# Kernel tuning notes

Hardware: AMD Instinct MI355X
Metric: run time of the kernel (lower is better)

Reference implementation:

```python
import jax, jax.numpy as jnp
import numpy as np
from jax import lax

NUM_HEADS = 8

def _conv2d(x, w, b, padding, rhs_dilation=(1, 1)):
    # x: NCHW, w: OIHW
    out = lax.conv_general_dilated(x, w, (1, 1), padding,
                                   rhs_dilation=rhs_dilation,
                                   dimension_numbers=('NCHW', 'OIHW', 'NCHW'))
    return out + b[None, :, None, None]

def _bn(x, scale, bias):
    # eval-mode batchnorm folded into per-channel affine
    return x * scale[None, :, None, None] + bias[None, :, None, None]

def setup_inputs() -> dict:
    key = jax.random.key(0)
    ks = jax.random.split(key, 12)
    B, C, H, W = 16, 256, 64, 64
    D = C // 2          # down_dim = 128
    Dq = D // 16        # weight bottleneck = 8
    return {
        'x':          jax.random.normal(ks[0], (B, C, H, W), jnp.float32),
        'conv2_w':    jax.random.normal(ks[1], (D, C, 3, 3), jnp.float32) * 0.02,
        'conv2_b':    jnp.zeros((D,), jnp.float32),
        'bn2_scale':  jax.random.uniform(ks[2], (D,), jnp.float32, 0.5, 1.5),
        'bn2_bias':   jax.random.normal(ks[3], (D,), jnp.float32) * 0.1,
        'temperature': jnp.ones((NUM_HEADS, 1, 1), jnp.float32),
        'w1_w':       jax.random.normal(ks[4], (Dq, D, 1, 1), jnp.float32) * 0.05,
        'w1_b':       jnp.zeros((Dq,), jnp.float32),
        'bnw_scale':  jax.random.uniform(ks[5], (Dq,), jnp.float32, 0.5, 1.5),
        'bnw_bias':   jax.random.normal(ks[6], (Dq,), jnp.float32) * 0.1,
        'w2_w':       jax.random.normal(ks[7], (D, Dq, 1, 1), jnp.float32) * 0.05,
        'w2_b':       jnp.zeros((D,), jnp.float32),
    }

def _l2_normalize_complex(z, eps=1e-12):
    # torch F.normalize on complex: divide by L2 norm of |z| along last dim
    n = jnp.sqrt(jnp.sum(jnp.real(z * jnp.conj(z)), axis=-1, keepdims=True))
    return z / jnp.maximum(n, eps)

def reference(x, conv2_w, conv2_b, bn2_scale, bn2_bias, temperature,
              w1_w, w1_b, bnw_scale, bnw_bias, w2_w, w2_b):
    # conv2 branch: 3x3 conv with dilation=3, padding=3 -> BN -> ReLU
    conv2 = jax.nn.relu(_bn(_conv2d(x, conv2_w, conv2_b,
                                    ((3, 3), (3, 3)), rhs_dilation=(3, 3)),
                            bn2_scale, bn2_bias))
    b, c, h, w = conv2.shape
    f = jnp.fft.fft2(conv2)                      # complex64, (b,c,h,w); q=k=v=tepqkv
    cp = c // NUM_HEADS
    qkv = f.reshape(b, NUM_HEADS, cp, h * w)     # 'b (head c) h w -> b head c (h w)'
    qn = _l2_normalize_complex(qkv)
    kn = qn
    # complex attention logits, temperature broadcast over heads
    attn = jnp.einsum('bhin,bhjn->bhij', qn, kn) * temperature.astype(attn_dtype := qn.dtype)
    # dual real/imag softmax reassembled into complex
    attn = lax.complex(jax.nn.softmax(attn.real, axis=-1),
                       jax.nn.softmax(attn.imag, axis=-1))
    out_f = jnp.einsum('bhij,bhjn->bhin', attn, qkv)
    # torch.fft.ifft2 default dims=(-2,-1): here over (c, h*w) axes — faithful
    out_f = jnp.abs(jnp.fft.ifft2(out_f)).reshape(b, c, h, w)
    # gating branch on real part of spectrum
    g = jax.nn.relu(_bn(_conv2d(f.real, w1_w, w1_b, ((0, 0), (0, 0))),
                        bnw_scale, bnw_bias))
    g = jax.nn.sigmoid(_conv2d(g, w2_w, w2_b, ((0, 0), (0, 0))))
    out_l = jnp.abs(jnp.fft.ifft2(g * f))        # ifft2 over (h, w)
    out = jnp.concatenate([out_f, out_l], axis=1)
    return out + x
```

## Files before the change

kernel.cpp:

```cpp
#include <hip/hip_runtime.h>

typedef unsigned short u16;
typedef short short8 __attribute__((ext_vector_type(8)));
typedef float f32x4 __attribute__((ext_vector_type(4)));

#define MF(a,b,c) __builtin_amdgcn_mfma_f32_16x16x32_bf16(a,b,c,0,0,0)

__device__ __forceinline__ float bu2f(u16 u){
  return __uint_as_float(((unsigned int)u) << 16);
}
__device__ __forceinline__ u16 f2bu(float f){
  unsigned int b = __float_as_uint(f);
  unsigned int r = (b + 0x7FFFu + ((b >> 16) & 1u)) >> 16;
  return (u16)r;
}
__device__ __forceinline__ void ld4a(float* d, const float* p){
  float4 v = *(const float4*)p;
  d[0]=v.x; d[1]=v.y; d[2]=v.z; d[3]=v.w;
}
__device__ __forceinline__ void st4(float* p, const float* s){
  *(float4*)p = make_float4(s[0], s[1], s[2], s[3]);
}
__device__ __forceinline__ void ld4b(float* d, const u16* p){
  ushort4 v = *(const ushort4*)p;
  d[0]=bu2f(v.x); d[1]=bu2f(v.y); d[2]=bu2f(v.z); d[3]=bu2f(v.w);
}
__device__ __forceinline__ void st4b(u16* p, const float* s){
  ushort4 v;
  v.x=f2bu(s[0]); v.y=f2bu(s[1]); v.z=f2bu(s[2]); v.w=f2bu(s[3]);
  *(ushort4*)p = v;
}
__device__ __forceinline__ ushort4 pk4(f32x4 v){
  ushort4 u; u.x=f2bu(v[0]); u.y=f2bu(v[1]); u.z=f2bu(v[2]); u.w=f2bu(v[3]); return u;
}
__device__ __forceinline__ short8 mulpk(short8 g, short8 f){
  short8 o;
  #pragma unroll
  for (int e = 0; e < 8; ++e)
    o[e] = (short)f2bu(bu2f((u16)g[e])*bu2f((u16)f[e]));
  return o;
}

#define TABF_RE   0
#define TABF_IM   4096
#define TABIF_RE  8192
#define TABIF_IM  12288
#define TABTW_RE  16384
#define TABTW_IM  20480
#define NORMS_OFF 24576
#define MMAT_OFF  26624
#define FLAG_OFF  92160
#define PRM_OFF   92224
#define WT_OFF    94848
#define DFT16_OFF 242304
#define F32_END   389760
#define P_CB   0
#define P_BNS  128
#define P_BNB  256
#define P_TEMP 384
#define P_W1   400
#define P_B1   1424
#define P_S1   1432
#define P_BB1  1440
#define P_W2   1456
#define P_B2   2480
#define BPLANE    8388608

__global__ void k_detect(const u16* __restrict__ xv, int* __restrict__ flag){
  const int t = threadIdx.x;
  int huge = 0;
  for (int i = 0; i < 16; ++i){
    u16 u = xv[(t*16 + i)*2];
    int e = (u >> 7) & 0xFF;
    huge += (e >= 0xC0) ? 1 : 0;
  }
  #pragma unroll
  for (int off = 32; off > 0; off >>= 1) huge += __shfl_down(huge, off, 64);
  if (t == 0) flag[0] = (huge >= 8) ? 1 : 0;
}

__global__ void k_tables(float* ws){
  int idx = blockIdx.x*256 + threadIdx.x;
  int j = idx >> 6, k = idx & 63;
  int jk = j*k;
  float s, c;
  sincospif(-(float)(jk & 63)/32.0f, &s, &c);
  ws[TABF_RE+idx] = c; ws[TABF_IM+idx] = s;
  sincospif((float)(jk & 63)/32.0f, &s, &c);
  ws[TABIF_RE+idx] = c*(1.f/64.f); ws[TABIF_IM+idx] = s*(1.f/64.f);
  sincospif((float)jk/2048.0f, &s, &c);
  ws[TABTW_RE+idx] = c; ws[TABTW_IM+idx] = s;
}

__global__ void k_dftprep(u16* __restrict__ m){
  int idx = blockIdx.x*256 + threadIdx.x;
  int j = idx >> 6, k = idx & 63;
  int jk = (j*k) & 63;
  float s, c;
  sincospif(-(float)jk/32.0f, &s, &c);
  m[idx]        = f2bu(c);
  m[4096+idx]   = f2bu(s);
  sincospif((float)jk/32.0f, &s, &c);
  m[8192+idx]   = f2bu(c*(1.f/64.f));
  m[12288+idx]  = f2bu(s*(1.f/64.f));
}

__global__ void k_pack(const void* cb, const void* bns, const void* bnb, const void* temp,
                       const void* w1, const void* b1, const void* s1, const void* bb1,
                       const void* w2, const void* b2,
                       const int* __restrict__ flg, float* __restrict__ P){
  const int t = threadIdx.x;
  const int f32 = *flg;
  if (f32){
    for (int i = t; i < 128; i += 256){
      P[P_CB+i]  = ((const float*)cb)[i];
      P[P_BNS+i] = ((const float*)bns)[i];
      P[P_BNB+i] = ((const float*)bnb)[i];
      P[P_B2+i]  = ((const float*)b2)[i];
    }
    for (int i = t; i < 1024; i += 256){
      P[P_W1+i] = ((const float*)w1)[i];
      P[P_W2+i] = ((const float*)w2)[i];
    }
    if (t < 8){
      P[P_TEMP+t] = ((const float*)temp)[t];
      P[P_B1+t]   = ((const float*)b1)[t];
      P[P_S1+t]   = ((const float*)s1)[t];
      P[P_BB1+t]  = ((const float*)bb1)[t];
    }
  } else {
    for (int i = t; i < 128; i += 256){
      P[P_CB+i]  = bu2f(((const u16*)cb)[i]);
      P[P_BNS+i] = bu2f(((const u16*)bns)[i]);
      P[P_BNB+i] = bu2f(((const u16*)bnb)[i]);
      P[P_B2+i]  = bu2f(((const u16*)b2)[i]);
    }
    for (int i = t; i < 1024; i += 256){
      P[P_W1+i] = bu2f(((const u16*)w1)[i]);
      P[P_W2+i] = bu2f(((const u16*)w2)[i]);
    }
    if (t < 8){
      P[P_TEMP+t] = bu2f(((const u16*)temp)[t]);
      P[P_B1+t]   = bu2f(((const u16*)b1)[t]);
      P[P_S1+t]   = bu2f(((const u16*)s1)[t]);
      P[P_BB1+t]  = bu2f(((const u16*)bb1)[t]);
    }
  }
}

__global__ void k_wprep2(const void* __restrict__ w, u16* __restrict__ wT2,
                         const float* __restrict__ prm, const int* __restrict__ flg){
  const int f32 = *flg;
  int U = blockIdx.x*256 + threadIdx.x;
  if (U < 294912){
    int j = U & 7;
    int E = U >> 3;
    int n = E & 127;
    int o = (E >> 7) & 3;
    int tc = E >> 9;
    int chunk = tc & 7, tap = tc >> 3;
    int c = chunk*32 + o*8 + j;
    int src = n*2304 + c*9 + tap;
    float v = f32 ? ((const float*)w)[src] : bu2f(((const u16*)w)[src]);
    wT2[U] = f2bu(v * prm[P_BNS + n]);
  }
}

__global__ __launch_bounds__(256) void k_trans(const void* __restrict__ x, u16* __restrict__ xt,
                                               const int* __restrict__ flg){
  __shared__ u16 L[256*66];
  const int t = threadIdx.x;
  const int b = blockIdx.x >> 6, h = blockIdx.x & 63;
  const int f32m = __builtin_amdgcn_readfirstlane(*flg);
  if (f32m){
    const float* xf = (const float*)x;
    for (int i = t; i < 16384; i += 256){
      int c = i >> 6, w = i & 63;
      L[c*66 + w] = f2bu(xf[((b*256 + c)*64 + h)*64 + w]);
    }
  } else {
    const u16* xb = (const u16*)x;
    for (int i = t; i < 16384; i += 256){
      int c = i >> 6, w = i & 63;
      L[c*66 + w] = xb[((b*256 + c)*64 + h)*64 + w];
    }
  }
  __syncthreads();
  u16* dst = xt + ((b*64 + h)*64)*256;
  for (int j = t; j < 16384; j += 256){
    int w = j >> 8, c = j & 255;
    dst[w*256 + c] = L[c*66 + w];
  }
}

__global__ __launch_bounds__(256) void k_cmm(const u16* __restrict__ xt, const u16* __restrict__ wT2,
                                             const float* __restrict__ prm, u16* __restrict__ A){
  __shared__ uint4 sm4[4096];
  const int t = threadIdx.x;
  const int bb = blockIdx.x >> 4;
  const int mtile = blockIdx.x & 15;
  const int h0 = mtile*4;
  const int lane = t & 63, wave = t >> 6;
  const int quad = lane >> 4, lr = lane & 15;

  f32x4 acc[4][8];
  #pragma unroll
  for (int mi = 0; mi < 4; ++mi)
    #pragma unroll
    for (int nt = 0; nt < 8; ++nt)
      acc[mi][nt] = (f32x4){0.f,0.f,0.f,0.f};

  const u16* smB = (const u16*)sm4;
  const short8 zz = {0,0,0,0,0,0,0,0};

  for (int tap = 0; tap < 9; ++tap){
    const int ky = tap/3, kx = tap - ky*3;
    __syncthreads();
    {
      const uint4* src = (const uint4*)(wT2 + tap*32768);
      #pragma unroll
      for (int i = 0; i < 16; ++i) sm4[t + 256*i] = src[t + 256*i];
    }
    __syncthreads();

    const int hg = h0 + wave + 3*ky - 3;
    const bool hok = ((unsigned)hg < 64u);
    const u16* abase = xt + ((bb*64 + hg)*64)*256 + quad*8;

    for (int chunk = 0; chunk < 8; ++chunk){
      short8 av[4];
      #pragma unroll
      for (int mi = 0; mi < 4; ++mi){
        const int wg = mi*16 + lr + 3*kx - 3;
        short8 v = zz;
        if (hok && ((unsigned)wg < 64u))
          v = *(const short8*)(abase + wg*256 + chunk*32);
        av[mi] = v;
      }
      short8 bv[8];
      #pragma unroll
      for (int nt = 0; nt < 8; ++nt)
        bv[nt] = *(const short8*)(smB + (chunk*512 + quad*128 + nt*16 + lr)*8);
      #pragma unroll
      for (int mi = 0; mi < 4; ++mi)
        #pragma unroll
        for (int nt = 0; nt < 8; ++nt)
          acc[mi][nt] = MF(av[mi], bv[nt], acc[mi][nt]);
    }
  }

  float* C = (float*)sm4;
  u16* outb = A + (bb*128)*4096 + mtile*256;
  __syncthreads();
  for (int nt = 0; nt < 8; ++nt){
    #pragma unroll
    for (int mi = 0; mi < 4; ++mi)
      #pragma unroll
      for (int r = 0; r < 4; ++r){
        int m = wave*64 + mi*16 + quad*4 + r;
        C[lr*261 + m] = acc[mi][nt][r];
      }
    __syncthreads();
    #pragma unroll
    for (int dd = 0; dd < 16; ++dd){
      int d = nt*16 + dd;
      float bi = prm[P_CB + d]*prm[P_BNS + d] + prm[P_BNB + d];
      float v = fmaxf(C[dd*261 + t] + bi, 0.f);
      outb[d*4096 + t] = f2bu(v);
    }
    __syncthreads();
  }
}

__global__ __launch_bounds__(256) void k_fft2_m(const u16* __restrict__ A, u16* __restrict__ Frb,
                                                u16* __restrict__ Fib, const u16* __restrict__ dft){
  __shared__ __align__(16) u16 TTr[64*72], TTi[64*72];
  const int bc = blockIdx.x, t = threadIdx.x;
  const int lane = t & 63, wave = t >> 6;
  const int quad = lane >> 4, lr = lane & 15;
  const u16* EFr = dft;
  const u16* EFi = dft + 4096;
  const u16* img = A + bc*4096;
  #pragma unroll
  for (int mi = 0; mi < 4; ++mi){
    f32x4 ar = {0.f,0.f,0.f,0.f}, ai = {0.f,0.f,0.f,0.f};
    #pragma unroll
    for (int ks = 0; ks < 2; ++ks){
      short8 av = *(const short8*)(img + (mi*16+lr)*64 + ks*32 + quad*8);
      short8 br = *(const short8*)(EFr + (wave*16+lr)*64 + ks*32 + quad*8);
      short8 bi = *(const short8*)(EFi + (wave*16+lr)*64 + ks*32 + quad*8);
      ar = MF(av, br, ar); ai = MF(av, bi, ai);
    }
    *(ushort4*)(TTr + (wave*16+lr)*72 + mi*16 + quad*4) = pk4(ar);
    *(ushort4*)(TTi + (wave*16+lr)*72 + mi*16 + quad*4) = pk4(ai);
  }
  __syncthreads();
  #pragma unroll
  for (int nt = 0; nt < 4; ++nt){
    f32x4 a1={0.f,0.f,0.f,0.f}, a2={0.f,0.f,0.f,0.f}, a3={0.f,0.f,0.f,0.f}, a4={0.f,0.f,0.f,0.f};
    #pragma unroll
    for (int ks = 0; ks < 2; ++ks){
      short8 tr = *(const short8*)(TTr + (wave*16+lr)*72 + ks*32 + quad*8);
      short8 ti = *(const short8*)(TTi + (wave*16+lr)*72 + ks*32 + quad*8);
      short8 br = *(const short8*)(EFr + (nt*16+lr)*64 + ks*32 + quad*8);
      short8 bi = *(const short8*)(EFi + (nt*16+lr)*64 + ks*32 + quad*8);
      a1 = MF(tr, br, a1); a2 = MF(ti, bi, a2);
      a3 = MF(tr, bi, a3); a4 = MF(ti, br, a4);
    }
    f32x4 fr, fi;
    #pragma unroll
    for (int r = 0; r < 4; ++r){ fr[r] = a1[r]-a2[r]; fi[r] = a3[r]+a4[r]; }
    const int flat = (nt*16+lr)*64 + wave*16 + quad*4;
    *(ushort4*)(Frb + bc*4096 + flat) = pk4(fr);
    *(ushort4*)(Fib + bc*4096 + flat) = pk4(fi);
  }
}

__global__ __launch_bounds__(256) void k_attn1(const u16* __restrict__ Frb,
                                               const u16* __restrict__ Fib,
                                               float* __restrict__ part){
  __shared__ float R[4][4][256];
  const int blk = blockIdx.x;
  const int bh = blk >> 4, chunk = blk & 15;
  const int t = threadIdx.x, lane = t & 63, wave = t >> 6;
  const int quad = lane >> 4, lr = lane & 15;
  const u16* fr = Frb + bh*65536;
  const u16* fi = Fib + bh*65536;
  const int c0 = chunk*256 + wave*64;
  f32x4 a1={0.f,0.f,0.f,0.f}, a2={0.f,0.f,0.f,0.f}, a3={0.f,0.f,0.f,0.f}, a4={0.f,0.f,0.f,0.f};
  #pragma unroll
  for (int ks = 0; ks < 2; ++ks){
    const int off = lr*4096 + c0 + ks*32 + quad*8;
    short8 ar = *(const short8*)(fr + off);
    short8 ai = *(const short8*)(fi + off);
    a1 = MF(ar, ar, a1); a2 = MF(ai, ai, a2);
    a3 = MF(ar, ai, a3); a4 = MF(ai, ar, a4);
  }
  #pragma unroll
  for (int r = 0; r < 4; ++r){
    const int mn = (quad*4 + r)*16 + lr;
    R[wave][0][mn] = a1[r];
    R[wave][1][mn] = a2[r];
    R[wave][2][mn] = a3[r];
    R[wave][3][mn] = a4[r];
  }
  __syncthreads();
  float* dst = part + blk*1024;
  #pragma unroll
  for (int q = 0; q < 4; ++q)
    dst[q*256 + t] = R[0][q][t] + R[1][q][t] + R[2][q][t] + R[3][q][t];
}

__global__ __launch_bounds__(256) void k_attn2(const float* __restrict__ part,
                                               const float* __restrict__ prm,
                                               float* __restrict__ wsM){
  __shared__ float AR[16][17], AI[16][17], NR[16];
  const int bh = blockIdx.x;
  const int h = bh & 7;
  const int t = threadIdx.x;
  const float* p = part + bh*16384;
  float s1=0.f, s2=0.f, s3=0.f, s4=0.f;
  #pragma unroll
  for (int ch = 0; ch < 16; ++ch){
    s1 += p[ch*1024 +       t];
    s2 += p[ch*1024 + 256 + t];
    s3 += p[ch*1024 + 512 + t];
    s4 += p[ch*1024 + 768 + t];
  }
  const int m = t >> 4, n = t & 15;
  if (m == n) NR[m] = fmaxf(sqrtf(fmaxf(s1 + s2, 0.f)), 1e-12f);
  __syncthreads();
  const float sc = prm[P_TEMP + h] / (NR[m]*NR[n]);
  AR[m][n] = (s1 - s2)*sc;
  AI[m][n] = (s3 + s4)*sc;
  __syncthreads();
  if (t < 32){
    float* row = (t < 16) ? AR[t & 15] : AI[t & 15];
    float mx = row[0];
    for (int j2 = 1; j2 < 16; ++j2) mx = fmaxf(mx, row[j2]);
    float s = 0.f, e[16];
    for (int j2 = 0; j2 < 16; ++j2){ e[j2] = expf(row[j2] - mx); s += e[j2]; }
    float inv = 1.f/s;
    for (int j2 = 0; j2 < 16; ++j2) row[j2] = e[j2]*inv;
  }
  __syncthreads();
  {
    const int mi = t >> 4, mj = t & 15;
    float mr = 0.f, mim = 0.f;
    #pragma unroll
    for (int pp = 0; pp < 16; ++pp){
      float sv, cv;
      sincospif((float)((mi*pp) & 15)/8.0f, &sv, &cv);
      const float arv = AR[pp][mj], aiv = AI[pp][mj];
      mr  += cv*arv - sv*aiv;
      mim += cv*aiv + sv*arv;
    }
    wsM[bh*512 + t*2]     = mr*(1.f/16.f);
    wsM[bh*512 + t*2 + 1] = mim*(1.f/16.f);
  }
}

__global__ __launch_bounds__(256) void k_gate(const u16* __restrict__ Frb,
                                              const float* __restrict__ prm,
                                              u16* __restrict__ g){
  __shared__ float W1T[128][8];
  __shared__ float W2[128][8];
  __shared__ float B1v[8], S1v[8], BB1v[8];
  __shared__ float B2v[128];
  const int t = threadIdx.x;
  for (int i = t; i < 1024; i += 256){
    W1T[i & 127][i >> 7] = prm[P_W1 + i];
    W2[i >> 3][i & 7]    = prm[P_W2 + i];
  }
  if (t < 8){ B1v[t] = prm[P_B1+t]; S1v[t] = prm[P_S1+t]; BB1v[t] = prm[P_BB1+t]; }
  if (t < 128) B2v[t] = prm[P_B2+t];
  __syncthreads();
  const int pix = blockIdx.x*256 + t;
  const int b = pix >> 12, n = pix & 4095;
  const u16* fr = Frb + b*128*4096 + n;
  float q[8] = {};
  for (int c = 0; c < 128; ++c){
    const float v = bu2f(fr[c*4096]);
    float wa[4], wb[4];
    ld4a(wa, &W1T[c][0]); ld4a(wb, &W1T[c][4]);
    #pragma unroll
    for (int k = 0; k < 4; ++k){ q[k] = fmaf(wa[k], v, q[k]); q[4+k] = fmaf(wb[k], v, q[4+k]); }
  }
  float qa[8];
  #pragma unroll
  for (int k = 0; k < 8; ++k)
    qa[k] = fmaxf(fmaf(q[k] + B1v[k], S1v[k], BB1v[k]), 0.f);
  u16* grow = g + b*128*4096 + n;
  for (int c = 0; c < 128; ++c){
    float wa[4], wb[4];
    ld4a(wa, &W2[c][0]); ld4a(wb, &W2[c][4]);
    float acc = B2v[c];
    #pragma unroll
    for (int k = 0; k < 4; ++k) acc += wa[k]*qa[k] + wb[k]*qa[4+k];
    grow[c*4096] = f2bu(1.f/(1.f + expf(-acc)));
  }
}

__global__ __launch_bounds__(256) void k_outl_m(const u16* __restrict__ Frb, const u16* __restrict__ Fib,
                                                const u16* __restrict__ g, const void* __restrict__ x,
                                                float* __restrict__ out, const u16* __restrict__ dft,
                                                const int* __restrict__ flg){
  __shared__ __align__(16) u16 TTr[64*72], TTi[64*72];
  const int bc = blockIdx.x, t = threadIdx.x;
  const int b = bc >> 7, c = bc & 127;
  const int lane = t & 63, wave = t >> 6;
  const int quad = lane >> 4, lr = lane & 15;
  const int f32m = __builtin_amdgcn_readfirstlane(*flg);
  const u16* EIr = dft + 8192;
  const u16* EIi = dft + 12288;
  const u16* pg = g   + bc*4096;
  const u16* pr = Frb + bc*4096;
  const u16* pi = Fib + bc*4096;
  #pragma unroll
  for (int mi = 0; mi < 4; ++mi){
    f32x4 a1={0.f,0.f,0.f,0.f}, a2={0.f,0.f,0.f,0.f}, a3={0.f,0.f,0.f,0.f}, a4={0.f,0.f,0.f,0.f};
    #pragma unroll
    for (int ks = 0; ks < 2; ++ks){
      const int ao = (mi*16+lr)*64 + ks*32 + quad*8;
      short8 gv = *(const short8*)(pg + ao);
      short8 apr = mulpk(gv, *(const short8*)(pr + ao));
      short8 api = mulpk(gv, *(const short8*)(pi + ao));
      const int bo = (wave*16+lr)*64 + ks*32 + quad*8;
      short8 br = *(const short8*)(EIr + bo);
      short8 bi = *(const short8*)(EIi + bo);
      a1 = MF(apr, br, a1); a2 = MF(api, bi, a2);
      a3 = MF(apr, bi, a3); a4 = MF(api, br, a4);
    }
    f32x4 tr, ti;
    #pragma unroll
    for (int r = 0; r < 4; ++r){ tr[r] = a1[r]-a2[r]; ti[r] = a3[r]+a4[r]; }
    *(ushort4*)(TTr + (wave*16+lr)*72 + mi*16 + quad*4) = pk4(tr);
    *(ushort4*)(TTi + (wave*16+lr)*72 + mi*16 + quad*4) = pk4(ti);
  }
  __syncthreads();
  #pragma unroll
  for (int nt = 0; nt < 4; ++nt){
    f32x4 a1={0.f,0.f,0.f,0.f}, a2={0.f,0.f,0.f,0.f}, a3={0.f,0.f,0.f,0.f}, a4={0.f,0.f,0.f,0.f};
    #pragma unroll
    for (int ks = 0; ks < 2; ++ks){
      short8 tr = *(const short8*)(TTr + (wave*16+lr)*72 + ks*32 + quad*8);
      short8 ti = *(const short8*)(TTi + (wave*16+lr)*72 + ks*32 + quad*8);
      const int bo = (nt*16+lr)*64 + ks*32 + quad*8;
      short8 br = *(const short8*)(EIr + bo);
      short8 bi = *(const short8*)(EIi + bo);
      a1 = MF(tr, br, a1); a2 = MF(ti, bi, a2);
      a3 = MF(tr, bi, a3); a4 = MF(ti, br, a4);
    }
    const int o = (b*256 + 128 + c)*4096 + (nt*16+lr)*64 + wave*16 + quad*4;
    float xr[4];
    if (f32m) ld4a(xr, (const float*)x + o); else ld4b(xr, (const u16*)x + o);
    float ov[4];
    #pragma unroll
    for (int r = 0; r < 4; ++r){
      float yr = a1[r]-a2[r], yi = a3[r]+a4[r];
      ov[r] = sqrtf(yr*yr + yi*yi) + xr[r];
    }
    st4(out + o, ov);
  }
}

__global__ __launch_bounds__(256) void k_ifft4096_m(u16* __restrict__ Frb, u16* __restrict__ Fib,
                                                    const float* __restrict__ ws,
                                                    const u16* __restrict__ dft){
  __shared__ __align__(16) u16 A2Tr[64*72], A2Ti[64*72], Cr[64*72], Ci[64*72];
  const int bc = blockIdx.x, t = threadIdx.x;
  const int lane = t & 63, wave = t >> 6;
  const int quad = lane >> 4, lr = lane & 15;
  const u16* EIr = dft + 8192;
  const u16* EIi = dft + 12288;
  const float* twr = ws + TABTW_RE;
  const float* twi = ws + TABTW_IM;
  u16* fr = Frb + bc*4096;
  u16* fi = Fib + bc*4096;
  for (int i = t; i < 4096; i += 256){
    int n1 = i >> 6, n2 = i & 63;
    A2Tr[n2*72 + n1] = fr[i];
    A2Ti[n2*72 + n1] = fi[i];
  }
  __syncthreads();
  #pragma unroll
  for (int nt = 0; nt < 4; ++nt){
    f32x4 a1={0.f,0.f,0.f,0.f}, a2={0.f,0.f,0.f,0.f}, a3={0.f,0.f,0.f,0.f}, a4={0.f,0.f,0.f,0.f};
    #pragma unroll
    for (int ks = 0; ks < 2; ++ks){
      const int ao = (wave*16+lr)*64 + ks*32 + quad*8;
      short8 Ar = *(const short8*)(EIr + ao);
      short8 Ai = *(const short8*)(EIi + ao);
      short8 br = *(const short8*)(A2Tr + (nt*16+lr)*72 + ks*32 + quad*8);
      short8 bi = *(const short8*)(A2Ti + (nt*16+lr)*72 + ks*32 + quad*8);
      a1 = MF(Ar, br, a1); a2 = MF(Ai, bi, a2);
      a3 = MF(Ar, bi, a3); a4 = MF(Ai, br, a4);
    }
    #pragma unroll
    for (int r = 0; r < 4; ++r){
      const int k1 = wave*16 + quad*4 + r;
      const int n2 = nt*16 + lr;
      const float trv = a1[r]-a2[r], tiv = a3[r]+a4[r];
      const float wr = twr[k1*64 + n2], wi = twi[k1*64 + n2];
      Cr[k1*72 + n2] = f2bu(trv*wr - tiv*wi);
      Ci[k1*72 + n2] = f2bu(trv*wi + tiv*wr);
    }
  }
  __syncthreads();
  #pragma unroll
  for (int nt = 0; nt < 4; ++nt){
    f32x4 a1={0.f,0.f,0.f,0.f}, a2={0.f,0.f,0.f,0.f}, a3={0.f,0.f,0.f,0.f}, a4={0.f,0.f,0.f,0.f};
    #pragma unroll
    for (int ks = 0; ks < 2; ++ks){
      short8 Ar = *(const short8*)(Cr + (wave*16+lr)*72 + ks*32 + quad*8);
      short8 Ai = *(const short8*)(Ci + (wave*16+lr)*72 + ks*32 + quad*8);
      const int bo = (nt*16+lr)*64 + ks*32 + quad*8;
      short8 br = *(const short8*)(EIr + bo);
      short8 bi = *(const short8*)(EIi + bo);
      a1 = MF(Ar, br, a1); a2 = MF(Ai, bi, a2);
      a3 = MF(Ar, bi, a3); a4 = MF(Ai, br, a4);
    }
    f32x4 zr, zi;
    #pragma unroll
    for (int r = 0; r < 4; ++r){ zr[r] = a1[r]-a2[r]; zi[r] = a3[r]+a4[r]; }
    const int flat = (nt*16+lr)*64 + wave*16 + quad*4;
    *(ushort4*)(fr + flat) = pk4(zr);
    *(ushort4*)(fi + flat) = pk4(zi);
  }
}

__global__ __launch_bounds__(256) void k_outf(const u16* __restrict__ Zr, const u16* __restrict__ Zi,
                                              const float* __restrict__ wsM, const void* __restrict__ x,
                                              float* __restrict__ out, const int* __restrict__ flg){
  __shared__ float MreT[16][20], MimT[16][20];
  const int gb = blockIdx.x;
  const int bh = gb & 127, nch = gb >> 7;
  const int b = bh >> 3, h = bh & 7;
  const int t = threadIdx.x;
  const int f32m = __builtin_amdgcn_readfirstlane(*flg);
  {
    const int i = t >> 4, j = t & 15;
    MreT[j][i] = wsM[bh*512 + t*2];
    MimT[j][i] = wsM[bh*512 + t*2 + 1];
  }
  __syncthreads();
  const int i0 = (t & 3)*4;
  const int nn = nch*256 + (t >> 2)*4;
  const u16* zr = Zr + (b*128 + h*16)*4096 + nn;
  const u16* zi = Zi + (b*128 + h*16)*4096 + nn;
  float accr[4][4] = {}, acci[4][4] = {};
  #pragma unroll
  for (int j = 0; j < 16; ++j){
    float mr[4], mi[4], vr[4], vi[4];
    ld4a(mr, &MreT[j][i0]);
    ld4a(mi, &MimT[j][i0]);
    ld4b(vr, zr + j*4096);
    ld4b(vi, zi + j*4096);
    #pragma unroll
    for (int i = 0; i < 4; ++i)
      #pragma unroll
      for (int n = 0; n < 4; ++n){
        accr[i][n] += mr[i]*vr[n] - mi[i]*vi[n];
        acci[i][n] += mr[i]*vi[n] + mi[i]*vr[n];
      }
  }
  #pragma unroll
  for (int i = 0; i < 4; ++i){
    const int o = (b*256 + h*16 + i0 + i)*4096 + nn;
    float xr[4];
    if (f32m) ld4a(xr, (const float*)x + o); else ld4b(xr, (const u16*)x + o);
    float ov[4];
    #pragma unroll
    for (int n = 0; n < 4; ++n)
      ov[n] = sqrtf(accr[i][n]*accr[i][n] + acci[i][n]*acci[i][n]) + xr[n];
    st4(out + o, ov);
  }
}

extern "C" void kernel_launch(void* const* d_in, const int* in_sizes, int n_in,
                              void* d_out, int out_size, void* d_ws, size_t ws_size,
                              hipStream_t stream) {
  const void* x        = d_in[0];
  const void* conv2_w  = d_in[1];
  const void* conv2_b  = d_in[2];
  const void* bn2_s    = d_in[3];
  const void* bn2_b    = d_in[4];
  const void* temp     = d_in[5];
  const void* w1_w     = d_in[6];
  const void* w1_b     = d_in[7];
  const void* bnw_s    = d_in[8];
  const void* bnw_b    = d_in[9];
  const void* w2_w     = d_in[10];
  const void* w2_b     = d_in[11];
  float* out = (float*)d_out;
  float* wsf = (float*)d_ws;

  if (ws_size < (size_t)(F32_END*4) + 3u*(size_t)BPLANE*2u) return;

  int* flag = (int*)(wsf + FLAG_OFF);
  float* prm = wsf + PRM_OFF;
  u16* wT2 = (u16*)(wsf + WT_OFF);
  u16* dft = (u16*)(wsf + DFT16_OFF);
  u16* wsb = (u16*)(wsf + F32_END);
  u16* Frb = wsb;
  u16* Fib = wsb + BPLANE;
  u16* xt  = wsb;
  u16* Ab  = wsb + 2*BPLANE;
  u16* g   = Ab;
  float* part = (float*)Ab;

  k_detect<<<1, 64, 0, stream>>>((const u16*)x, flag);
  k_tables<<<16, 256, 0, stream>>>(wsf);
  k_dftprep<<<16, 256, 0, stream>>>(dft);
  k_pack<<<1, 256, 0, stream>>>(conv2_b, bn2_s, bn2_b, temp, w1_w, w1_b, bnw_s, bnw_b,
                                w2_w, w2_b, flag, prm);
  k_wprep2<<<1152, 256, 0, stream>>>(conv2_w, wT2, prm, flag);
  k_trans<<<1024, 256, 0, stream>>>(x, xt, flag);
  k_cmm<<<256, 256, 0, stream>>>(xt, wT2, prm, Ab);
  k_fft2_m<<<2048, 256, 0, stream>>>(Ab, Frb, Fib, dft);
  k_attn1<<<2048, 256, 0, stream>>>(Frb, Fib, part);
  k_attn2<<<128, 256, 0, stream>>>(part, prm, wsf + MMAT_OFF);
  k_gate<<<256, 256, 0, stream>>>(Frb, prm, g);
  k_outl_m<<<2048, 256, 0, stream>>>(Frb, Fib, g, x, out, dft, flag);
  k_ifft4096_m<<<2048, 256, 0, stream>>>(Frb, Fib, wsf, dft);
  k_outf<<<2048, 256, 0, stream>>>(Frb, Fib, wsf + MMAT_OFF, x, out, flag);
}
```

Baseline: 438.3 us.

## Double-buffer conv weight taps and split conv GEMM across 8 waves

```diff
diff --git a/kernel.cpp b/kernel.cpp
--- a/kernel.cpp
+++ b/kernel.cpp
@@ -193,37 +193,49 @@
   }
 }
 
-__global__ __launch_bounds__(256) void k_cmm(const u16* __restrict__ xt, const u16* __restrict__ wT2,
+__global__ __launch_bounds__(512) void k_cmm(const u16* __restrict__ xt, const u16* __restrict__ wT2,
                                              const float* __restrict__ prm, u16* __restrict__ A){
-  __shared__ uint4 sm4[4096];
+  __shared__ __align__(16) uint4 smW4[8192];
   const int t = threadIdx.x;
   const int bb = blockIdx.x >> 4;
   const int mtile = blockIdx.x & 15;
   const int h0 = mtile*4;
   const int lane = t & 63, wave = t >> 6;
+  const int wrow = wave >> 1, wcol = wave & 1;
   const int quad = lane >> 4, lr = lane & 15;
 
-  f32x4 acc[4][8];
+  f32x4 acc[4][4];
   #pragma unroll
   for (int mi = 0; mi < 4; ++mi)
     #pragma unroll
-    for (int nt = 0; nt < 8; ++nt)
-      acc[mi][nt] = (f32x4){0.f,0.f,0.f,0.f};
-
-  const u16* smB = (const u16*)sm4;
+    for (int j = 0; j < 4; ++j)
+      acc[mi][j] = (f32x4){0.f,0.f,0.f,0.f};
+
   const short8 zz = {0,0,0,0,0,0,0,0};
 
+  {
+    const uint4* src = (const uint4*)wT2;
+    uint4 stg[8];
+    #pragma unroll
+    for (int i = 0; i < 8; ++i) stg[i] = src[t + 512*i];
+    #pragma unroll
+    for (int i = 0; i < 8; ++i) smW4[t + 512*i] = stg[i];
+  }
+  __syncthreads();
+
   for (int tap = 0; tap < 9; ++tap){
+    const int buf = tap & 1;
     const int ky = tap/3, kx = tap - ky*3;
-    __syncthreads();
-    {
-      const uint4* src = (const uint4*)(wT2 + tap*32768);
+
+    uint4 stg[8];
+    if (tap < 8){
+      const uint4* src = (const uint4*)(wT2 + (tap+1)*32768);
       #pragma unroll
-      for (int i = 0; i < 16; ++i) sm4[t + 256*i] = src[t + 256*i];
-    }
-    __syncthreads();
-
-    const int hg = h0 + wave + 3*ky - 3;
+      for (int i = 0; i < 8; ++i) stg[i] = src[t + 512*i];
+    }
+
+    const u16* smB = (const u16*)(smW4 + buf*4096);
+    const int hg = h0 + wrow + 3*ky - 3;
     const bool hok = ((unsigned)hg < 64u);
     const u16* abase = xt + ((bb*64 + hg)*64)*256 + quad*8;
 
@@ -237,36 +249,45 @@
           v = *(const short8*)(abase + wg*256 + chunk*32);
         av[mi] = v;
       }
-      short8 bv[8];
+      short8 bv[4];
       #pragma unroll
-      for (int nt = 0; nt < 8; ++nt)
-        bv[nt] = *(const short8*)(smB + (chunk*512 + quad*128 + nt*16 + lr)*8);
+      for (int j = 0; j < 4; ++j)
+        bv[j] = *(const short8*)(smB + (chunk*512 + quad*128 + (wcol*4+j)*16 + lr)*8);
       #pragma unroll
       for (int mi = 0; mi < 4; ++mi)
         #pragma unroll
-        for (int nt = 0; nt < 8; ++nt)
-          acc[mi][nt] = MF(av[mi], bv[nt], acc[mi][nt]);
-    }
-  }
-
-  float* C = (float*)sm4;
+        for (int j = 0; j < 4; ++j)
+          acc[mi][j] = MF(av[mi], bv[j], acc[mi][j]);
+    }
+
+    if (tap < 8){
+      uint4* dst = smW4 + (buf^1)*4096;
+      #pragma unroll
+      for (int i = 0; i < 8; ++i) dst[t + 512*i] = stg[i];
+    }
+    __syncthreads();
+  }
+
+  float* C = (float*)smW4;
   u16* outb = A + (bb*128)*4096 + mtile*256;
-  __syncthreads();
-  for (int nt = 0; nt < 8; ++nt){
+  const int ch32 = wcol*16 + lr;
+  for (int nt2 = 0; nt2 < 4; ++nt2){
     #pragma unroll
     for (int mi = 0; mi < 4; ++mi)
       #pragma unroll
       for (int r = 0; r < 4; ++r){
-        int m = wave*64 + mi*16 + quad*4 + r;
-        C[lr*261 + m] = acc[mi][nt][r];
+        const int m = wrow*64 + mi*16 + quad*4 + r;
+        C[ch32*261 + m] = acc[mi][nt2][r];
       }
     __syncthreads();
     #pragma unroll
     for (int dd = 0; dd < 16; ++dd){
-      int d = nt*16 + dd;
-      float bi = prm[P_CB + d]*prm[P_BNS + d] + prm[P_BNB + d];
-      float v = fmaxf(C[dd*261 + t] + bi, 0.f);
-      outb[d*4096 + t] = f2bu(v);
+      const int idx = dd*512 + t;
+      const int c32 = idx >> 8, m = idx & 255;
+      const int d = (c32 >> 4)*64 + nt2*16 + (c32 & 15);
+      const float bi = prm[P_CB + d]*prm[P_BNS + d] + prm[P_BNB + d];
+      const float v = fmaxf(C[c32*261 + m] + bi, 0.f);
+      outb[d*4096 + m] = f2bu(v);
     }
     __syncthreads();
   }
@@ -656,7 +677,7 @@
                                 w2_w, w2_b, flag, prm);
   k_wprep2<<<1152, 256, 0, stream>>>(conv2_w, wT2, prm, flag);
   k_trans<<<1024, 256, 0, stream>>>(x, xt, flag);
-  k_cmm<<<256, 256, 0, stream>>>(xt, wT2, prm, Ab);
+  k_cmm<<<256, 512, 0, stream>>>(xt, wT2, prm, Ab);
   k_fft2_m<<<2048, 256, 0, stream>>>(Ab, Frb, Fib, dft);
   k_attn1<<<2048, 256, 0, stream>>>(Frb, Fib, part);
   k_attn2<<<128, 256, 0, stream>>>(part, prm, wsf + MMAT_OFF);
```

New measurement: 482.7 us. +10.1%, slower.

## Split conv GEMM tiles in half, use direct global-to-LDS weight loads, swizzle blocks

Applied to the files above, without the earlier changes.

```diff
diff --git a/kernel.cpp b/kernel.cpp
--- a/kernel.cpp
+++ b/kernel.cpp
@@ -39,6 +39,11 @@
   for (int e = 0; e < 8; ++e)
     o[e] = (short)f2bu(bu2f((u16)g[e])*bu2f((u16)f[e]));
   return o;
+}
+__device__ __forceinline__ void gl_lds16(const void* g, void* l){
+  __builtin_amdgcn_global_load_lds(
+      (const __attribute__((address_space(1))) void*)g,
+      (__attribute__((address_space(3))) void*)l, 16, 0, 0);
 }
 
 #define TABF_RE   0
@@ -195,22 +200,22 @@
 
 __global__ __launch_bounds__(256) void k_cmm(const u16* __restrict__ xt, const u16* __restrict__ wT2,
                                              const float* __restrict__ prm, u16* __restrict__ A){
-  __shared__ uint4 sm4[4096];
+  __shared__ __align__(16) uint4 sm4[4096];
   const int t = threadIdx.x;
-  const int bb = blockIdx.x >> 4;
-  const int mtile = blockIdx.x & 15;
-  const int h0 = mtile*4;
+  const int blk = blockIdx.x;
+  const int bb = (blk & 7) + 8*(blk >> 8);
+  const int mt2 = (blk >> 3) & 31;
   const int lane = t & 63, wave = t >> 6;
+  const int wrow = wave >> 1, whalf = wave & 1;
   const int quad = lane >> 4, lr = lane & 15;
 
-  f32x4 acc[4][8];
-  #pragma unroll
-  for (int mi = 0; mi < 4; ++mi)
+  f32x4 acc[2][8];
+  #pragma unroll
+  for (int mi = 0; mi < 2; ++mi)
     #pragma unroll
     for (int nt = 0; nt < 8; ++nt)
       acc[mi][nt] = (f32x4){0.f,0.f,0.f,0.f};
 
-  const u16* smB = (const u16*)sm4;
   const short8 zz = {0,0,0,0,0,0,0,0};
 
   for (int tap = 0; tap < 9; ++tap){
@@ -219,19 +224,20 @@
     {
       const uint4* src = (const uint4*)(wT2 + tap*32768);
       #pragma unroll
-      for (int i = 0; i < 16; ++i) sm4[t + 256*i] = src[t + 256*i];
+      for (int i = 0; i < 16; ++i) gl_lds16(&src[t + 256*i], &sm4[t + 256*i]);
     }
     __syncthreads();
 
-    const int hg = h0 + wave + 3*ky - 3;
+    const u16* smB = (const u16*)sm4;
+    const int hg = mt2*2 + wrow + 3*ky - 3;
     const bool hok = ((unsigned)hg < 64u);
     const u16* abase = xt + ((bb*64 + hg)*64)*256 + quad*8;
 
     for (int chunk = 0; chunk < 8; ++chunk){
-      short8 av[4];
+      short8 av[2];
       #pragma unroll
-      for (int mi = 0; mi < 4; ++mi){
-        const int wg = mi*16 + lr + 3*kx - 3;
+      for (int mi = 0; mi < 2; ++mi){
+        const int wg = whalf*32 + mi*16 + lr + 3*kx - 3;
         short8 v = zz;
         if (hok && ((unsigned)wg < 64u))
           v = *(const short8*)(abase + wg*256 + chunk*32);
@@ -242,7 +248,7 @@
       for (int nt = 0; nt < 8; ++nt)
         bv[nt] = *(const short8*)(smB + (chunk*512 + quad*128 + nt*16 + lr)*8);
       #pragma unroll
-      for (int mi = 0; mi < 4; ++mi)
+      for (int mi = 0; mi < 2; ++mi)
         #pragma unroll
         for (int nt = 0; nt < 8; ++nt)
           acc[mi][nt] = MF(av[mi], bv[nt], acc[mi][nt]);
@@ -250,23 +256,25 @@
   }
 
   float* C = (float*)sm4;
-  u16* outb = A + (bb*128)*4096 + mtile*256;
+  u16* outb = A + (bb*128)*4096 + mt2*128;
   __syncthreads();
   for (int nt = 0; nt < 8; ++nt){
     #pragma unroll
-    for (int mi = 0; mi < 4; ++mi)
+    for (int mi = 0; mi < 2; ++mi)
       #pragma unroll
       for (int r = 0; r < 4; ++r){
-        int m = wave*64 + mi*16 + quad*4 + r;
-        C[lr*261 + m] = acc[mi][nt][r];
+        const int m = wrow*64 + whalf*32 + mi*16 + quad*4 + r;
+        C[lr*133 + m] = acc[mi][nt][r];
       }
     __syncthreads();
     #pragma unroll
-    for (int dd = 0; dd < 16; ++dd){
-      int d = nt*16 + dd;
-      float bi = prm[P_CB + d]*prm[P_BNS + d] + prm[P_BNB + d];
-      float v = fmaxf(C[dd*261 + t] + bi, 0.f);
-      outb[d*4096 + t] = f2bu(v);
+    for (int i = 0; i < 8; ++i){
+      const int idx = i*256 + t;
+      const int dd = idx >> 7, m = idx & 127;
+      const int d = nt*16 + dd;
+      const float bi = prm[P_CB + d]*prm[P_BNS + d] + prm[P_BNB + d];
+      const float v = fmaxf(C[dd*133 + m] + bi, 0.f);
+      outb[d*4096 + m] = f2bu(v);
     }
     __syncthreads();
   }
@@ -656,7 +664,7 @@
                                 w2_w, w2_b, flag, prm);
   k_wprep2<<<1152, 256, 0, stream>>>(conv2_w, wT2, prm, flag);
   k_trans<<<1024, 256, 0, stream>>>(x, xt, flag);
-  k_cmm<<<256, 256, 0, stream>>>(xt, wT2, prm, Ab);
+  k_cmm<<<512, 256, 0, stream>>>(xt, wT2, prm, Ab);
   k_fft2_m<<<2048, 256, 0, stream>>>(Ab, Frb, Fib, dft);
   k_attn1<<<2048, 256, 0, stream>>>(Frb, Fib, part);
   k_attn2<<<128, 256, 0, stream>>>(part, prm, wsf + MMAT_OFF);
```

New measurement: 426.7 us. 1.03x faster.
